# Performance work log

Measured on AMD Instinct MI355X. Metric: run time of the kernel, lower is better.

The kernel has to match this reference:

```python
import jax, jax.numpy as jnp
import numpy as np

B = 50000      # batch of target nodes
N = 200000     # total nodes in feature table
K = 32         # sampled neighbors per node
F = 256        # feature dim
F_OUT = 256    # output dim


def setup_inputs() -> dict:
    key = jax.random.key(0)
    k1, k2, k3, k4, k5 = jax.random.split(key, 5)
    x_self = jax.random.normal(k1, (B, F), dtype=jnp.float32)
    feats = jax.random.normal(k2, (N, F), dtype=jnp.float32)
    neigh_idx = jax.random.randint(k3, (B, K), 0, N, dtype=jnp.int64)
    # Linear(2F -> F_OUT), stored as (in, out) for x @ W
    W = jax.random.normal(k4, (F_OUT, 2 * F), dtype=jnp.float32) * (1.0 / np.sqrt(2 * F))
    W = W.T  # (2F, F_OUT)
    b = jax.random.normal(k5, (F_OUT,), dtype=jnp.float32) * 0.01
    return {"x_self": x_self, "feats": feats, "neigh_idx": neigh_idx, "W": W, "b": b}


def reference(x_self, feats, neigh_idx, W, b):
    # gather neighbor features: [B, K, F]
    neigh_feats = feats[neigh_idx]
    # MeanAggregator: mean over neighbor axis (-2)
    x_neigh = neigh_feats.mean(axis=-2)            # [B, F]
    # concat=True path: cat([x_self, x_neigh], axis=1) -> [B, 2F]
    h = jnp.concatenate([x_self, x_neigh], axis=1)
    # Linear layer
    return h @ W + b                                # [B, F_OUT]
```

## Files before the change

### kernel.cpp

```cpp
#include <hip/hip_runtime.h>
#include <hip/hip_bf16.h>
#include <stdint.h>

#define NB 50000
#define NN 200000
#define KN 32
#define FD 256
#define F2 512
#define FO 256

typedef __attribute__((ext_vector_type(8))) short short8v;
typedef __attribute__((ext_vector_type(4))) short short4v;
typedef __attribute__((ext_vector_type(4))) float floatx4;
typedef __attribute__((ext_vector_type(2))) float float2v;

__device__ inline short f2bf(float f) {
    __hip_bfloat16 h = __float2bfloat16(f);
    return *reinterpret_cast<short*>(&h);
}

__global__ void k_quant_feats(const float* __restrict__ feats,
                              unsigned char* __restrict__ Q) {
    long t = (long)blockIdx.x * blockDim.x + threadIdx.x;
    long base = t * 8;
    const float4* src = (const float4*)(feats + base);
    float4 a = src[0], b = src[1];
    int lo = 0, hi = 0;
    lo = __builtin_amdgcn_cvt_pk_fp8_f32(a.x, a.y, lo, false);
    lo = __builtin_amdgcn_cvt_pk_fp8_f32(a.z, a.w, lo, true);
    hi = __builtin_amdgcn_cvt_pk_fp8_f32(b.x, b.y, hi, false);
    hi = __builtin_amdgcn_cvt_pk_fp8_f32(b.z, b.w, hi, true);
    int2 o = { lo, hi };
    *(int2*)(Q + base) = o;
}

__global__ void k_swizzle_W(const float* __restrict__ W,
                            __hip_bfloat16* __restrict__ Wsw) {
    int u = blockIdx.x * blockDim.x + threadIdx.x;
    if (u >= 16384) return;
    int c = u >> 10;
    int t = (u >> 6) & 15;
    int l = u & 63;
    int kq = (l >> 4) * 8;
    int n  = t * 16 + (l & 15);
    short o[8];
#pragma unroll
    for (int j = 0; j < 8; ++j)
        o[j] = f2bf(W[(long)(c * 32 + kq + j) * FO + n]);
    *(short8v*)((short*)Wsw + (long)u * 8) = *(short8v*)o;
}

__global__ void k_gather_mean(const unsigned char* __restrict__ Q,
                              const int* __restrict__ idx,
                              __hip_bfloat16* __restrict__ Hn) {
    int wave = threadIdx.x >> 6;
    int lane = threadIdx.x & 63;
    int b = blockIdx.x * 4 + wave;
    int cl   = lane & 15;
    int quad = lane >> 4;

    const int* ib = idx + (long)b * KN;
    float2v acc2[8];
#pragma unroll
    for (int j = 0; j < 8; ++j) acc2[j] = (float2v)(0.f);

#pragma unroll
    for (int k = 0; k < 8; ++k) {
        int nid = ib[4 * k + quad];
        int4 v = *(const int4*)(Q + (long)nid * FD + cl * 16);
        acc2[0] += __builtin_amdgcn_cvt_pk_f32_fp8(v.x, false);
        acc2[1] += __builtin_amdgcn_cvt_pk_f32_fp8(v.x, true);
        acc2[2] += __builtin_amdgcn_cvt_pk_f32_fp8(v.y, false);
        acc2[3] += __builtin_amdgcn_cvt_pk_f32_fp8(v.y, true);
        acc2[4] += __builtin_amdgcn_cvt_pk_f32_fp8(v.z, false);
        acc2[5] += __builtin_amdgcn_cvt_pk_f32_fp8(v.z, true);
        acc2[6] += __builtin_amdgcn_cvt_pk_f32_fp8(v.w, false);
        acc2[7] += __builtin_amdgcn_cvt_pk_f32_fp8(v.w, true);
    }

#pragma unroll
    for (int j = 0; j < 8; ++j) {
        acc2[j].x += __shfl_xor(acc2[j].x, 16);
        acc2[j].y += __shfl_xor(acc2[j].y, 16);
        acc2[j].x += __shfl_xor(acc2[j].x, 32);
        acc2[j].y += __shfl_xor(acc2[j].y, 32);
    }

    float2v p0 = (quad & 1) ? acc2[2] : acc2[0];
    float2v p1 = (quad & 1) ? acc2[3] : acc2[1];
    float2v q0 = (quad & 1) ? acc2[6] : acc2[4];
    float2v q1 = (quad & 1) ? acc2[7] : acc2[5];
    float2v s0 = (quad & 2) ? q0 : p0;
    float2v s1 = (quad & 2) ? q1 : p1;
    const float s = 1.0f / (float)KN;
    short o[4] = { f2bf(s0.x * s), f2bf(s0.y * s), f2bf(s1.x * s), f2bf(s1.y * s) };
    *(short4v*)((short*)Hn + (long)b * FD + cl * 16 + quad * 4) = *(short4v*)o;
}

__global__ void __launch_bounds__(128, 2)
k_gemm(const float* __restrict__ x_self,
       const __hip_bfloat16* __restrict__ Hn,
       const __hip_bfloat16* __restrict__ Wsw,
       const float* __restrict__ bias,
       float* __restrict__ out) {
    int wave = threadIdx.x >> 6;
    int lane = threadIdx.x & 63;
    int cl   = lane & 15;
    int quad = lane >> 4;
    int kq   = quad * 8;

    int mf = blockIdx.x * 64 + wave * 32;
    long r0 = min(mf + cl, NB - 1);
    long r1 = min(mf + 16 + cl, NB - 1);

    floatx4 acc[2][16];
#pragma unroll
    for (int f = 0; f < 2; ++f)
#pragma unroll
        for (int t = 0; t < 16; ++t) acc[f][t] = (floatx4)(0.f);

    const short8v* wp = (const short8v*)Wsw;

#pragma unroll
    for (int c = 0; c < 8; ++c) {
        float4 p0 = *(const float4*)(x_self + r0 * FD + c * 32 + kq);
        float4 p1 = *(const float4*)(x_self + r0 * FD + c * 32 + kq + 4);
        float4 p2 = *(const float4*)(x_self + r1 * FD + c * 32 + kq);
        float4 p3 = *(const float4*)(x_self + r1 * FD + c * 32 + kq + 4);
        short a0s[8] = { f2bf(p0.x), f2bf(p0.y), f2bf(p0.z), f2bf(p0.w),
                         f2bf(p1.x), f2bf(p1.y), f2bf(p1.z), f2bf(p1.w) };
        short a1s[8] = { f2bf(p2.x), f2bf(p2.y), f2bf(p2.z), f2bf(p2.w),
                         f2bf(p3.x), f2bf(p3.y), f2bf(p3.z), f2bf(p3.w) };
        short8v a0 = *(short8v*)a0s;
        short8v a1 = *(short8v*)a1s;
#pragma unroll
        for (int t = 0; t < 16; ++t) {
            short8v bf = wp[(c * 16 + t) * 64 + lane];
            acc[0][t] = __builtin_amdgcn_mfma_f32_16x16x32_bf16(a0, bf, acc[0][t], 0, 0, 0);
            acc[1][t] = __builtin_amdgcn_mfma_f32_16x16x32_bf16(a1, bf, acc[1][t], 0, 0, 0);
        }
    }

#pragma unroll
    for (int c = 0; c < 8; ++c) {
        short8v a0 = *(const short8v*)((const short*)Hn + r0 * FD + c * 32 + kq);
        short8v a1 = *(const short8v*)((const short*)Hn + r1 * FD + c * 32 + kq);
#pragma unroll
        for (int t = 0; t < 16; ++t) {
            short8v bf = wp[((c + 8) * 16 + t) * 64 + lane];
            acc[0][t] = __builtin_amdgcn_mfma_f32_16x16x32_bf16(a0, bf, acc[0][t], 0, 0, 0);
            acc[1][t] = __builtin_amdgcn_mfma_f32_16x16x32_bf16(a1, bf, acc[1][t], 0, 0, 0);
        }
    }

#pragma unroll
    for (int t = 0; t < 16; ++t) {
        int n = t * 16 + cl;
        float bv = bias[n];
#pragma unroll
        for (int f = 0; f < 2; ++f) {
            int row = mf + f * 16 + quad * 4;
#pragma unroll
            for (int r = 0; r < 4; ++r) {
                if (row + r < NB)
                    out[(long)(row + r) * FO + n] = acc[f][t][r] + bv;
            }
        }
    }
}

extern "C" void kernel_launch(void* const* d_in, const int* in_sizes, int n_in,
                              void* d_out, int out_size, void* d_ws, size_t ws_size,
                              hipStream_t stream) {
    const float* x_self = (const float*)d_in[0];
    const float* feats  = (const float*)d_in[1];
    const int*   idx    = (const int*)d_in[2];
    const float* W      = (const float*)d_in[3];
    const float* bias   = (const float*)d_in[4];
    float* out = (float*)d_out;

    unsigned char*  Q   = (unsigned char*)d_ws;
    __hip_bfloat16* Hn  = (__hip_bfloat16*)((char*)d_ws + (size_t)NN * FD);
    __hip_bfloat16* Wsw = (__hip_bfloat16*)((char*)d_ws + (size_t)NN * FD
                                                        + (size_t)NB * FD * 2);

    k_quant_feats<<<NN * FD / 8 / 256, 256, 0, stream>>>(feats, Q);
    k_swizzle_W<<<64, 256, 0, stream>>>(W, Wsw);
    k_gather_mean<<<NB / 4, 256, 0, stream>>>(Q, idx, Hn);
    k_gemm<<<(NB + 63) / 64, 128, 0, stream>>>(x_self, Hn, Wsw, bias, out);
}
```

Measured before the change: 428.6 us.

## Fuse neighbor gather-mean into GEMM via LDS and merge prep kernels

```diff
diff --git a/kernel.cpp b/kernel.cpp
--- a/kernel.cpp
+++ b/kernel.cpp
@@ -9,6 +9,8 @@
 #define F2 512
 #define FO 256
 
+#define QUANT_BLOCKS (NN * FD / 8 / 256)
+
 typedef __attribute__((ext_vector_type(8))) short short8v;
 typedef __attribute__((ext_vector_type(4))) short short4v;
 typedef __attribute__((ext_vector_type(4))) float floatx4;
@@ -19,99 +21,97 @@
     return *reinterpret_cast<short*>(&h);
 }
 
-__global__ void k_quant_feats(const float* __restrict__ feats,
-                              unsigned char* __restrict__ Q) {
-    long t = (long)blockIdx.x * blockDim.x + threadIdx.x;
-    long base = t * 8;
-    const float4* src = (const float4*)(feats + base);
-    float4 a = src[0], b = src[1];
-    int lo = 0, hi = 0;
-    lo = __builtin_amdgcn_cvt_pk_fp8_f32(a.x, a.y, lo, false);
-    lo = __builtin_amdgcn_cvt_pk_fp8_f32(a.z, a.w, lo, true);
-    hi = __builtin_amdgcn_cvt_pk_fp8_f32(b.x, b.y, hi, false);
-    hi = __builtin_amdgcn_cvt_pk_fp8_f32(b.z, b.w, hi, true);
-    int2 o = { lo, hi };
-    *(int2*)(Q + base) = o;
+__global__ void k_prep(const float* __restrict__ feats,
+                       unsigned char* __restrict__ Q,
+                       const float* __restrict__ W,
+                       __hip_bfloat16* __restrict__ Wsw) {
+    int bx = blockIdx.x;
+    if (bx < QUANT_BLOCKS) {
+        long t = (long)bx * 256 + threadIdx.x;
+        long base = t * 8;
+        const float4* src = (const float4*)(feats + base);
+        float4 a = src[0], b = src[1];
+        int lo = 0, hi = 0;
+        lo = __builtin_amdgcn_cvt_pk_fp8_f32(a.x, a.y, lo, false);
+        lo = __builtin_amdgcn_cvt_pk_fp8_f32(a.z, a.w, lo, true);
+        hi = __builtin_amdgcn_cvt_pk_fp8_f32(b.x, b.y, hi, false);
+        hi = __builtin_amdgcn_cvt_pk_fp8_f32(b.z, b.w, hi, true);
+        int2 o = { lo, hi };
+        *(int2*)(Q + base) = o;
+    } else {
+        int u = (bx - QUANT_BLOCKS) * 256 + threadIdx.x;
+        int c = u >> 10;
+        int t = (u >> 6) & 15;
+        int l = u & 63;
+        int kq = (l >> 4) * 8;
+        int n  = t * 16 + (l & 15);
+        short o[8];
+#pragma unroll
+        for (int j = 0; j < 8; ++j)
+            o[j] = f2bf(W[(long)(c * 32 + kq + j) * FO + n]);
+        *(short8v*)((short*)Wsw + (long)u * 8) = *(short8v*)o;
+    }
 }
 
-__global__ void k_swizzle_W(const float* __restrict__ W,
-                            __hip_bfloat16* __restrict__ Wsw) {
-    int u = blockIdx.x * blockDim.x + threadIdx.x;
-    if (u >= 16384) return;
-    int c = u >> 10;
-    int t = (u >> 6) & 15;
-    int l = u & 63;
-    int kq = (l >> 4) * 8;
-    int n  = t * 16 + (l & 15);
-    short o[8];
+__global__ void __launch_bounds__(256, 2)
+k_fused(const unsigned char* __restrict__ Q,
+        const int* __restrict__ idx,
+        const float* __restrict__ x_self,
+        const __hip_bfloat16* __restrict__ Wsw,
+        const float* __restrict__ bias,
+        float* __restrict__ out) {
+    __shared__ short hn[128 * 256];
+
+    const int wave = threadIdx.x >> 6;
+    const int lane = threadIdx.x & 63;
+    const int cl   = lane & 15;
+    const int quad = lane >> 4;
+    char* hnb = (char*)hn;
+
+    const float s = 1.0f / (float)KN;
+    const int wbase = cl * 32 + quad * 8;
+#pragma unroll 2
+    for (int tt = 0; tt < 32; ++tt) {
+        const int rloc = wave * 32 + tt;
+        const long b = min((int)(blockIdx.x * 128) + rloc, NB - 1);
+        const int* ib = idx + b * KN;
+        float2v acc2[8];
 #pragma unroll
-    for (int j = 0; j < 8; ++j)
-        o[j] = f2bf(W[(long)(c * 32 + kq + j) * FO + n]);
-    *(short8v*)((short*)Wsw + (long)u * 8) = *(short8v*)o;
-}
-
-__global__ void k_gather_mean(const unsigned char* __restrict__ Q,
-                              const int* __restrict__ idx,
-                              __hip_bfloat16* __restrict__ Hn) {
-    int wave = threadIdx.x >> 6;
-    int lane = threadIdx.x & 63;
-    int b = blockIdx.x * 4 + wave;
-    int cl   = lane & 15;
-    int quad = lane >> 4;
-
-    const int* ib = idx + (long)b * KN;
-    float2v acc2[8];
+        for (int j = 0; j < 8; ++j) acc2[j] = (float2v)(0.f);
 #pragma unroll
-    for (int j = 0; j < 8; ++j) acc2[j] = (float2v)(0.f);
-
+        for (int k = 0; k < 8; ++k) {
+            int nid = ib[4 * k + quad];
+            int4 v = *(const int4*)(Q + (long)nid * FD + cl * 16);
+            acc2[0] += __builtin_amdgcn_cvt_pk_f32_fp8(v.x, false);
+            acc2[1] += __builtin_amdgcn_cvt_pk_f32_fp8(v.x, true);
+            acc2[2] += __builtin_amdgcn_cvt_pk_f32_fp8(v.y, false);
+            acc2[3] += __builtin_amdgcn_cvt_pk_f32_fp8(v.y, true);
+            acc2[4] += __builtin_amdgcn_cvt_pk_f32_fp8(v.z, false);
+            acc2[5] += __builtin_amdgcn_cvt_pk_f32_fp8(v.z, true);
+            acc2[6] += __builtin_amdgcn_cvt_pk_f32_fp8(v.w, false);
+            acc2[7] += __builtin_amdgcn_cvt_pk_f32_fp8(v.w, true);
+        }
 #pragma unroll
-    for (int k = 0; k < 8; ++k) {
-        int nid = ib[4 * k + quad];
-        int4 v = *(const int4*)(Q + (long)nid * FD + cl * 16);
-        acc2[0] += __builtin_amdgcn_cvt_pk_f32_fp8(v.x, false);
-        acc2[1] += __builtin_amdgcn_cvt_pk_f32_fp8(v.x, true);
-        acc2[2] += __builtin_amdgcn_cvt_pk_f32_fp8(v.y, false);
-        acc2[3] += __builtin_amdgcn_cvt_pk_f32_fp8(v.y, true);
-        acc2[4] += __builtin_amdgcn_cvt_pk_f32_fp8(v.z, false);
-        acc2[5] += __builtin_amdgcn_cvt_pk_f32_fp8(v.z, true);
-        acc2[6] += __builtin_amdgcn_cvt_pk_f32_fp8(v.w, false);
-        acc2[7] += __builtin_amdgcn_cvt_pk_f32_fp8(v.w, true);
+        for (int j = 0; j < 8; ++j) {
+            acc2[j].x += __shfl_xor(acc2[j].x, 16);
+            acc2[j].y += __shfl_xor(acc2[j].y, 16);
+            acc2[j].x += __shfl_xor(acc2[j].x, 32);
+            acc2[j].y += __shfl_xor(acc2[j].y, 32);
+        }
+        float2v p0 = (quad & 1) ? acc2[2] : acc2[0];
+        float2v p1 = (quad & 1) ? acc2[3] : acc2[1];
+        float2v q0 = (quad & 1) ? acc2[6] : acc2[4];
+        float2v q1 = (quad & 1) ? acc2[7] : acc2[5];
+        float2v s0 = (quad & 2) ? q0 : p0;
+        float2v s1 = (quad & 2) ? q1 : p1;
+        short o[4] = { f2bf(s0.x * s), f2bf(s0.y * s), f2bf(s1.x * s), f2bf(s1.y * s) };
+        *(short4v*)(hnb + rloc * 512 + (wbase ^ ((tt & 7) << 4))) = *(short4v*)o;
     }
 
-#pragma unroll
-    for (int j = 0; j < 8; ++j) {
-        acc2[j].x += __shfl_xor(acc2[j].x, 16);
-        acc2[j].y += __shfl_xor(acc2[j].y, 16);
-        acc2[j].x += __shfl_xor(acc2[j].x, 32);
-        acc2[j].y += __shfl_xor(acc2[j].y, 32);
-    }
-
-    float2v p0 = (quad & 1) ? acc2[2] : acc2[0];
-    float2v p1 = (quad & 1) ? acc2[3] : acc2[1];
-    float2v q0 = (quad & 1) ? acc2[6] : acc2[4];
-    float2v q1 = (quad & 1) ? acc2[7] : acc2[5];
-    float2v s0 = (quad & 2) ? q0 : p0;
-    float2v s1 = (quad & 2) ? q1 : p1;
-    const float s = 1.0f / (float)KN;
-    short o[4] = { f2bf(s0.x * s), f2bf(s0.y * s), f2bf(s1.x * s), f2bf(s1.y * s) };
-    *(short4v*)((short*)Hn + (long)b * FD + cl * 16 + quad * 4) = *(short4v*)o;
-}
-
-__global__ void __launch_bounds__(128, 2)
-k_gemm(const float* __restrict__ x_self,
-       const __hip_bfloat16* __restrict__ Hn,
-       const __hip_bfloat16* __restrict__ Wsw,
-       const float* __restrict__ bias,
-       float* __restrict__ out) {
-    int wave = threadIdx.x >> 6;
-    int lane = threadIdx.x & 63;
-    int cl   = lane & 15;
-    int quad = lane >> 4;
-    int kq   = quad * 8;
-
-    int mf = blockIdx.x * 64 + wave * 32;
-    long r0 = min(mf + cl, NB - 1);
-    long r1 = min(mf + 16 + cl, NB - 1);
+    const int mf = (int)(blockIdx.x * 128) + wave * 32;
+    const long r0 = min(mf + cl, NB - 1);
+    const long r1 = min(mf + 16 + cl, NB - 1);
+    const int kq = quad * 8;
 
     floatx4 acc[2][16];
 #pragma unroll
@@ -141,10 +141,14 @@
         }
     }
 
+    const int ra = wave * 32 + cl;
+    const int rb = ra + 16;
+    const int rkey = (cl & 7) << 4;
 #pragma unroll
     for (int c = 0; c < 8; ++c) {
-        short8v a0 = *(const short8v*)((const short*)Hn + r0 * FD + c * 32 + kq);
-        short8v a1 = *(const short8v*)((const short*)Hn + r1 * FD + c * 32 + kq);
+        int coff = (c * 64 + quad * 16) ^ rkey;
+        short8v a0 = *(const short8v*)(hnb + ra * 512 + coff);
+        short8v a1 = *(const short8v*)(hnb + rb * 512 + coff);
 #pragma unroll
         for (int t = 0; t < 16; ++t) {
             short8v bf = wp[((c + 8) * 16 + t) * 64 + lane];
@@ -180,12 +184,8 @@
     float* out = (float*)d_out;
 
     unsigned char*  Q   = (unsigned char*)d_ws;
-    __hip_bfloat16* Hn  = (__hip_bfloat16*)((char*)d_ws + (size_t)NN * FD);
-    __hip_bfloat16* Wsw = (__hip_bfloat16*)((char*)d_ws + (size_t)NN * FD
-                                                        + (size_t)NB * FD * 2);
+    __hip_bfloat16* Wsw = (__hip_bfloat16*)((char*)d_ws + (size_t)NN * FD);
 
-    k_quant_feats<<<NN * FD / 8 / 256, 256, 0, stream>>>(feats, Q);
-    k_swizzle_W<<<64, 256, 0, stream>>>(W, Wsw);
-    k_gather_mean<<<NB / 4, 256, 0, stream>>>(Q, idx, Hn);
-    k_gemm<<<(NB + 63) / 64, 128, 0, stream>>>(x_self, Hn, Wsw, bias, out);
+    k_prep<<<QUANT_BLOCKS + 64, 256, 0, stream>>>(feats, Q, W, Wsw);
+    k_fused<<<(NB + 127) / 128, 256, 0, stream>>>(Q, idx, x_self, Wsw, bias, out);
 }
```

Result: slower. 547.3 us (+27.7%).
